# Performance work log

Measured on AMD Instinct MI355X. Metric: run time of the kernel, lower is better.

Reference implementation:

```python
import jax, jax.numpy as jnp
import numpy as np

IH, IW = 32, 32
HEADS, DIM_HEAD = 8, 32
EPS = 1e-6


def conv3x3(x, w):
    # x: [B,C,H,W], w: [O,I,3,3], stride 1, pad 1, no bias
    return jax.lax.conv_general_dilated(x, w, (1, 1), ((1, 1), (1, 1)),
                                        dimension_numbers=('NCHW', 'OIHW', 'NCHW'))


def groupnorm1(x, g, b):
    # GroupNorm(1, C): normalize over (C,H,W) per sample
    mu = jnp.mean(x, axis=(1, 2, 3), keepdims=True)
    var = jnp.var(x, axis=(1, 2, 3), keepdims=True)
    xn = (x - mu) * jax.lax.rsqrt(var + EPS)
    return xn * g[None, :, None, None] + b[None, :, None, None]


def proj(x, w, g, b):
    return jax.nn.gelu(groupnorm1(conv3x3(x, w), g, b), approximate=False)


def relative_index(ih, iw):
    coords = np.stack(np.meshgrid(np.arange(ih), np.arange(iw), indexing='ij')).reshape(2, -1)
    rel = coords[:, :, None] - coords[:, None, :]  # [2, n, n]
    rel[0] += ih - 1
    rel[1] += iw - 1
    rel[0] *= 2 * iw - 1
    return jnp.asarray(rel.sum(0).reshape(-1))  # [n*n]


def setup_inputs() -> dict:
    key = jax.random.key(0)
    ks = jax.random.split(key, 9)
    C = HEADS * DIM_HEAD  # 256
    B = 8
    s = 0.02
    inp = {
        'x': jax.random.normal(ks[0], (B, C, IH, IW), jnp.float32),
        'wq': jax.random.normal(ks[1], (C, C, 3, 3), jnp.float32) * s,
        'wk': jax.random.normal(ks[2], (C, C, 3, 3), jnp.float32) * s,
        'wv': jax.random.normal(ks[3], (C, C, 3, 3), jnp.float32) * s,
        'gq': jnp.ones((C,), jnp.float32), 'bq': jnp.zeros((C,), jnp.float32),
        'gk': jnp.ones((C,), jnp.float32), 'bk': jnp.zeros((C,), jnp.float32),
        'gv': jnp.ones((C,), jnp.float32), 'bv': jnp.zeros((C,), jnp.float32),
        'bias_table': jax.random.normal(ks[4], ((2 * IH - 1) * (2 * IW - 1), HEADS), jnp.float32) * s,
        'wo': jax.random.normal(ks[5], (C, C), jnp.float32) * s,
        'bo': jnp.zeros((C,), jnp.float32),
    }
    return inp


def reference(x, wq, wk, wv, gq, bq, gk, bk, gv, bv, bias_table, wo, bo):
    B, C, ih, iw = x.shape
    n = ih * iw
    h, d = HEADS, DIM_HEAD

    q = proj(x, wq, gq, bq)  # [B,C,H,W]
    k = proj(x, wk, gk, bk)
    v = proj(x, wv, gv, bv)

    # 'b c ih iw -> b (ih iw) c' then 'b n (h d) -> b h n d'  ==  [B,h,d,n] -> [B,h,n,d]
    def to_heads(t):
        return t.reshape(B, h, d, n).transpose(0, 1, 3, 2)

    q4, k4, v4 = to_heads(q), to_heads(k), to_heads(v)

    # NOTE: original code applies self.scale only when y is not None; y=None here -> no scale.
    dots = jnp.einsum('bhnd,bhmd->bhnm', q4, k4)  # [B,h,n,n]

    rel_idx = relative_index(ih, iw)  # [n*n]
    rel_bias = bias_table[rel_idx].reshape(n, n, h).transpose(2, 0, 1)[None]  # [1,h,n,n]

    attn = jax.nn.softmax(dots + rel_bias, axis=-1)
    out = jnp.einsum('bhnm,bhmd->bhnd', attn, v4)  # [B,h,n,d]

    # 'b h n d -> b n (h d)' then 'b (ih iw) c -> b c ih iw'
    out = out.transpose(0, 2, 1, 3).reshape(B, n, C).transpose(0, 2, 1).reshape(B, C, ih, iw)

    # to_out: 1x1 conv with bias (dropout=0 in eval)
    out = jnp.einsum('oc,bchw->bohw', wo, out) + bo[None, :, None, None]
    return out
```

## Files before the change

kernel.cpp:

```cpp
#include <hip/hip_runtime.h>
#include <cstdint>
#include <cstddef>

#define GEPS 1e-6f

using bf16x8 = __attribute__((ext_vector_type(8))) short;
using f32x4  = __attribute__((ext_vector_type(4))) float;

__device__ inline ushort f2bf(float x) {
    union { float f; uint32_t u; } v; v.f = x;
    uint32_t r = (v.u + 0x7fffu + ((v.u >> 16) & 1u)) >> 16;
    return (ushort)r;
}
__device__ inline float bf2f(ushort b) {
    union { float f; uint32_t u; } v; v.u = ((uint32_t)b) << 16;
    return v.f;
}

__device__ inline void gll16(const void* g, void* l) {
    __builtin_amdgcn_global_load_lds(
        (const __attribute__((address_space(1))) void*)g,
        (__attribute__((address_space(3))) void*)l, 16, 0, 0);
}

__global__ __launch_bounds__(256) void prep_k(
    const float* __restrict__ x,
    const float* __restrict__ wq, const float* __restrict__ wk,
    const float* __restrict__ wv, const float* __restrict__ wo,
    const float* __restrict__ btab,
    ushort* __restrict__ Ab, ushort* __restrict__ Wbuf,
    ushort* __restrict__ wo_bf, ushort* __restrict__ Bx)
{
    __shared__ __align__(16) ushort Xs[3 * 34 * 128];
    int tid = threadIdx.x;
    int blk = blockIdx.x;

    if (blk < 512) {
        int b = blk >> 6, py = (blk >> 1) & 31, half = blk & 1;
#pragma unroll
        for (int p = tid; p < 768; p += 256) {
            int yy = p >> 8;
            int q = p & 255;
            int col = (q >> 7) ? 33 : 0;
            int ci = q & 127;
            Xs[(yy * 34 + col) * 128 + ci] = 0;
        }
#pragma unroll
        for (int it = 0; it < 12; ++it) {
            int j = it * 256 + tid;
            int ci_l = j / 24;
            int o = (j - ci_l * 24) * 4;
            int yy = o >> 5, xx = o & 31;
            int row = py - 1 + yy;
            float4 v = make_float4(0.f, 0.f, 0.f, 0.f);
            if (row >= 0 && row < 32)
                v = *(const float4*)&x[((size_t)(b * 256 + half * 128 + ci_l)) * 1024 + row * 32 + xx];
            int base = (yy * 34 + xx + 1) * 128 + ci_l;
            Xs[base + 0 * 128] = f2bf(v.x);
            Xs[base + 1 * 128] = f2bf(v.y);
            Xs[base + 2 * 128] = f2bf(v.z);
            Xs[base + 3 * 128] = f2bf(v.w);
        }
        __syncthreads();
        ushort* dst = Ab + (size_t)(b * 1024 + py * 32) * 2304;
#pragma unroll
        for (int it = 0; it < 18; ++it) {
            int idx = it * 256 + tid;
            int ci8l = idx & 15;
            int tp = (idx >> 4) % 9;
            int px = idx / 144;
            int kh = tp / 3, kw = tp - kh * 3;
            uint4 p = *(const uint4*)&Xs[(kh * 34 + px + kw) * 128 + ci8l * 8];
            *(uint4*)&dst[(size_t)(px * 288 + tp * 32 + half * 16 + ci8l) * 8] = p;
        }
        return;
    }
    if (blk < 1280) {
        int wrow = blk - 512;
        int proj = wrow >> 8, co = wrow & 255;
        const float* src = ((proj == 0) ? wq : ((proj == 1) ? wk : wv)) + (size_t)co * 2304;
#pragma unroll
        for (int j = 0; j < 9; ++j) {
            int idx = j * 256 + tid;
            Xs[idx] = f2bf(src[idx]);
        }
        __syncthreads();
        ushort* dst = Wbuf + (size_t)wrow * 2304;
#pragma unroll
        for (int j = 0; j < 9; ++j)
            dst[j * 256 + tid] = Xs[tid * 9 + j];
        return;
    }
    if (blk < 1344) {
        int t = (blk - 1280) * 256 + tid;
        float4 v = *(const float4*)&wo[(size_t)t * 4];
        union { uint2 u; ushort s[4]; } o;
        o.s[0] = f2bf(v.x); o.s[1] = f2bf(v.y); o.s[2] = f2bf(v.z); o.s[3] = f2bf(v.w);
        *(uint2*)&wo_bf[(size_t)t * 4] = o.u;
        return;
    }
    int g = (blk - 1344) * 4 + (tid >> 6);
    int l = tid & 63;
    int h = g >> 10, qt = (g >> 4) & 63, kt = g & 15;
    int quad = l >> 4, c = l & 15;
    union { uint4 v[2]; ushort s[16]; } o;
#pragma unroll
    for (int f = 0; f < 4; ++f)
#pragma unroll
        for (int r = 0; r < 4; ++r) {
            int qrow = qt * 16 + quad * 4 + r;
            int key = kt * 64 + f * 16 + c;
            int dy = (qrow >> 5) - (key >> 5) + 31;
            int dx = (qrow & 31) - (key & 31) + 31;
            o.s[f * 4 + r] = f2bf(btab[(dy * 63 + dx) * 8 + h]);
        }
    uint4* dst = (uint4*)(Bx + ((size_t)g * 64 + l) * 16);
    dst[0] = o.v[0];
    dst[1] = o.v[1];
}

__global__ __launch_bounds__(256, 3) void gemm_bt(
    const ushort* __restrict__ A, const ushort* __restrict__ B,
    int M, int N, int K,
    ushort* __restrict__ Cpart,
    float* __restrict__ Cout, const float* __restrict__ bias, int mode)
{
    __shared__ __align__(16) ushort As[128 * 64];
    __shared__ __align__(16) ushort Bs[128 * 64];
    int tid = threadIdx.x;
    int mbase = blockIdx.x * 128, nbase = blockIdx.y * 128;
    int kspan = K / gridDim.z;
    int k0 = blockIdx.z * kspan;
    int wave = tid >> 6, lane = tid & 63;
    int wm = wave & 1, wn = wave >> 1;
    int quad = lane >> 4, c = lane & 15;

    int row_s = tid >> 3;
    int cc8 = (tid & 7) ^ (row_s & 7);
    ushort* ldsA = As + wave * 512;
    ushort* ldsB = Bs + wave * 512;

    f32x4 acc[4][4];
#pragma unroll
    for (int i = 0; i < 4; ++i)
#pragma unroll
        for (int j = 0; j < 4; ++j) acc[i][j] = (f32x4){0.f, 0.f, 0.f, 0.f};

    for (int kb = k0; kb < k0 + kspan; kb += 64) {
        __syncthreads();
#pragma unroll
        for (int R = 0; R < 4; ++R) {
            int row = R * 32 + row_s;
            gll16(A + (size_t)(mbase + row) * K + kb + cc8 * 8,
                  ldsA + R * 2048);
            gll16(B + (size_t)(nbase + row) * K + kb + cc8 * 8,
                  ldsB + R * 2048);
        }
        __syncthreads();
#pragma unroll
        for (int kq = 0; kq < 2; ++kq) {
            bf16x8 af[4], bfr[4];
            int sw = ((kq * 4 + quad) ^ (c & 7)) * 8;
#pragma unroll
            for (int i = 0; i < 4; ++i) {
                af[i]  = *(const bf16x8*)&As[(wm * 64 + i * 16 + c) * 64 + sw];
                bfr[i] = *(const bf16x8*)&Bs[(wn * 64 + i * 16 + c) * 64 + sw];
            }
#pragma unroll
            for (int i = 0; i < 4; ++i)
#pragma unroll
                for (int j = 0; j < 4; ++j)
                    acc[i][j] = __builtin_amdgcn_mfma_f32_16x16x32_bf16(
                        af[i], bfr[j], acc[i][j], 0, 0, 0);
        }
    }

    if (mode == 0) {
        ushort* Cp = Cpart + (size_t)blockIdx.z * M * N;
#pragma unroll
        for (int i = 0; i < 4; ++i) {
            int mrow = mbase + wm * 64 + i * 16 + quad * 4;
#pragma unroll
            for (int j = 0; j < 4; ++j) {
                int ncol = nbase + wn * 64 + j * 16 + c;
#pragma unroll
                for (int r = 0; r < 4; ++r)
                    Cp[(size_t)(mrow + r) * N + ncol] = f2bf(acc[i][j][r]);
            }
        }
    } else {
#pragma unroll
        for (int i = 0; i < 4; ++i) {
            int mrow0 = mbase + wm * 64 + i * 16 + quad * 4;
#pragma unroll
            for (int j = 0; j < 4; ++j) {
                int ncol = nbase + wn * 64 + j * 16 + c;
                int bb = ncol >> 10, px = ncol & 1023;
#pragma unroll
                for (int r = 0; r < 4; ++r) {
                    int o = mrow0 + r;
                    Cout[((size_t)bb * 256 + o) * 1024 + px] = acc[i][j][r] + bias[o];
                }
            }
        }
    }
}

__global__ __launch_bounds__(256) void stats1_k(const ushort* __restrict__ P0,
                                                const ushort* __restrict__ P1,
                                                float2* __restrict__ part)
{
    int t = blockIdx.x * 256 + threadIdx.x;
    size_t base = (size_t)t * 8;
    union { uint4 v; ushort s[8]; } a, b2;
    a.v  = *(const uint4*)&P0[base];
    b2.v = *(const uint4*)&P1[base];
    float s1 = 0.f, s2 = 0.f;
#pragma unroll
    for (int e = 0; e < 8; ++e) {
        float v = bf2f(a.s[e]) + bf2f(b2.s[e]);
        s1 += v; s2 += v * v;
    }
#pragma unroll
    for (int mk = 1; mk < 32; mk <<= 1) {
        s1 += __shfl_xor(s1, mk, 64);
        s2 += __shfl_xor(s2, mk, 64);
    }
    if ((threadIdx.x & 31) == 0) {
        int gg = t >> 5;
        int m = gg / 3;
        int proj = gg - m * 3;
        int b = m >> 10, slot = m & 1023;
        part[(proj * 8 + b) * 1024 + slot] = make_float2(s1, s2);
    }
}

__global__ __launch_bounds__(256) void stats2_k(const float2* __restrict__ part,
                                                float* __restrict__ stats)
{
    __shared__ float w1[4], w2[4];
    int s = blockIdx.x, tid = threadIdx.x;
    float s1 = 0.f, s2 = 0.f;
#pragma unroll
    for (int i = 0; i < 4; ++i) {
        float2 v = part[(size_t)s * 1024 + tid * 4 + i];
        s1 += v.x; s2 += v.y;
    }
#pragma unroll
    for (int mk = 1; mk < 64; mk <<= 1) {
        s1 += __shfl_xor(s1, mk, 64);
        s2 += __shfl_xor(s2, mk, 64);
    }
    if ((tid & 63) == 0) { w1[tid >> 6] = s1; w2[tid >> 6] = s2; }
    __syncthreads();
    if (tid == 0) {
        stats[s * 2 + 0] = w1[0] + w1[1] + w1[2] + w1[3];
        stats[s * 2 + 1] = w2[0] + w2[1] + w2[2] + w2[3];
    }
}

__global__ void gn_k(const ushort* __restrict__ P0, const ushort* __restrict__ P1,
                     const float* __restrict__ stats,
                     const float* __restrict__ gq, const float* __restrict__ bq,
                     const float* __restrict__ gk, const float* __restrict__ bk,
                     const float* __restrict__ gv, const float* __restrict__ bv,
                     ushort* __restrict__ qb, ushort* __restrict__ kb2,
                     ushort* __restrict__ vx)
{
    int t = blockIdx.x * 256 + threadIdx.x;
    int m = t / 96;
    int nn = (t - m * 96) * 8;
    int proj = nn >> 8, co = nn & 255;
    int b = m >> 10, px = m & 1023;
    float s1 = stats[(proj * 8 + b) * 2 + 0];
    float s2 = stats[(proj * 8 + b) * 2 + 1];
    const float Ninv = 1.f / 262144.f;
    float mu = s1 * Ninv;
    float var = fmaxf(s2 * Ninv - mu * mu, 0.f);
    float rsig = rsqrtf(var + GEPS);
    const float* gam = (proj == 0) ? gq : ((proj == 1) ? gk : gv);
    const float* bet = (proj == 0) ? bq : ((proj == 1) ? bk : bv);

    size_t base = (size_t)m * 768 + nn;
    union { uint4 v; ushort s[8]; } a, c2;
    a.v  = *(const uint4*)&P0[base];
    c2.v = *(const uint4*)&P1[base];
    union { uint4 v; ushort s[8]; } outp;
#pragma unroll
    for (int e = 0; e < 8; ++e) {
        int cc = co + e;
        float xv = bf2f(a.s[e]) + bf2f(c2.s[e]);
        float xn = (xv - mu) * rsig * gam[cc] + bet[cc];
        float ge = 0.5f * xn * (1.f + erff(xn * 0.70710678118654752f));
        outp.s[e] = f2bf(ge);
    }
    int h = co >> 5, d = co & 31;
    if (proj == 0) {
        *(uint4*)(qb + ((((size_t)b * 8 + h) * 1024 + px) * 32 + d)) = outp.v;
    } else if (proj == 1) {
        *(uint4*)(kb2 + ((((size_t)b * 8 + h) * 1024 + px) * 32 + d)) = outp.v;
    } else {
        ushort* vb = vx + ((size_t)b * 8 + h) * 32768;
        int kca = px >> 5, quad = (px >> 3) & 3, j = px & 7;
#pragma unroll
        for (int e = 0; e < 8; ++e) {
            int dd = d + e;
            vb[(((kca * 2 + (dd >> 4)) * 64) + quad * 16 + (dd & 15)) * 8 + j] = outp.s[e];
        }
    }
}

__global__ __launch_bounds__(256, 8) void attn_k(
    const ushort* __restrict__ qb, const ushort* __restrict__ kb,
    const ushort* __restrict__ vx, const ushort* __restrict__ Bx,
    ushort* __restrict__ Opart, float* __restrict__ lpart)
{
    __shared__ __align__(16) ushort Pl[4 * 16 * 72];
    int tid = threadIdx.x, wave = tid >> 6, lane = tid & 63;
    int quad = lane >> 4, c = lane & 15;
    int bh = blockIdx.y;
    int h = bh & 7;
    int z = blockIdx.z;
    int qbase = blockIdx.x * 64 + wave * 16;

    const ushort* Q  = qb + (size_t)bh * 1024 * 32;
    const ushort* Kp = kb + (size_t)bh * 1024 * 32;
    const ushort* Vb = vx + (size_t)bh * 32768;
    const ushort* bxp = Bx + (((size_t)(h * 64 + (qbase >> 4)) * 16) * 64 + lane) * 16;
    ushort* Pw = Pl + wave * 16 * 72;

    bf16x8 qf = *(const bf16x8*)&Q[(qbase + c) * 32 + quad * 8];

    float l_[4] = {0.f, 0.f, 0.f, 0.f};
    f32x4 Of0 = {0.f, 0.f, 0.f, 0.f}, Of1 = {0.f, 0.f, 0.f, 0.f};

    for (int kb64 = z * 512; kb64 < z * 512 + 512; kb64 += 64) {
        f32x4 S[4];
        f32x4 zf = {0.f, 0.f, 0.f, 0.f};
#pragma unroll
        for (int f = 0; f < 4; ++f) {
            bf16x8 kf = *(const bf16x8*)&Kp[(kb64 + f * 16 + c) * 32 + quad * 8];
            S[f] = __builtin_amdgcn_mfma_f32_16x16x32_bf16(qf, kf, zf, 0, 0, 0);
        }
        union { uint4 v[2]; ushort s[16]; } bu;
        const uint4* bsrc = (const uint4*)(bxp + (size_t)(kb64 >> 6) * 1024);
        bu.v[0] = bsrc[0];
        bu.v[1] = bsrc[1];
#pragma unroll
        for (int f = 0; f < 4; ++f)
#pragma unroll
            for (int r = 0; r < 4; ++r) {
                float p = __expf(S[f][r] + bf2f(bu.s[f * 4 + r]));
                S[f][r] = p;
                l_[r] += p;
            }
#pragma unroll
        for (int f = 0; f < 4; ++f)
#pragma unroll
            for (int r = 0; r < 4; ++r)
                Pw[(quad * 4 + r) * 72 + f * 16 + c] = f2bf(S[f][r]);
#pragma unroll
        for (int kc = 0; kc < 2; ++kc) {
            int kca = (kb64 >> 5) + kc;
            bf16x8 pf = *(const bf16x8*)&Pw[c * 72 + kc * 32 + quad * 8];
            bf16x8 vf0 = *(const bf16x8*)&Vb[((kca * 2 + 0) * 64 + lane) * 8];
            Of0 = __builtin_amdgcn_mfma_f32_16x16x32_bf16(pf, vf0, Of0, 0, 0, 0);
            bf16x8 vf1 = *(const bf16x8*)&Vb[((kca * 2 + 1) * 64 + lane) * 8];
            Of1 = __builtin_amdgcn_mfma_f32_16x16x32_bf16(pf, vf1, Of1, 0, 0, 0);
        }
    }
#pragma unroll
    for (int r = 0; r < 4; ++r) {
        float l = l_[r];
        l += __shfl_xor(l, 1, 64);
        l += __shfl_xor(l, 2, 64);
        l += __shfl_xor(l, 4, 64);
        l += __shfl_xor(l, 8, 64);
        int qr = qbase + quad * 4 + r;
        size_t ob = (((size_t)z * 64 + bh) * 1024 + qr) * 32;
        Opart[ob + c]      = f2bf(Of0[r]);
        Opart[ob + 16 + c] = f2bf(Of1[r]);
        if (c == 0) lpart[(size_t)z * 65536 + bh * 1024 + qr] = l;
    }
}

__global__ __launch_bounds__(256) void combine_k(const ushort* __restrict__ Opart,
                                                 const float* __restrict__ lpart,
                                                 ushort* __restrict__ attnout)
{
    int t = blockIdx.x * 256 + threadIdx.x;
    int g = t & 3;
    int qg = t >> 2;
    int bh = qg >> 10, qr = qg & 1023;
    int b = bh >> 3, h = bh & 7;
    size_t ob = ((size_t)qg) * 32 + g * 8;
    union { uint4 v; ushort s[8]; } o0, o1;
    o0.v = *(const uint4*)&Opart[ob];
    o1.v = *(const uint4*)&Opart[(size_t)64 * 1024 * 32 + ob];
    float inv = 1.f / (lpart[qg] + lpart[65536 + qg]);
    union { uint4 u; ushort s[8]; } o;
#pragma unroll
    for (int e = 0; e < 8; ++e)
        o.s[e] = f2bf((bf2f(o0.s[e]) + bf2f(o1.s[e])) * inv);
    *(uint4*)&attnout[(((size_t)b * 1024 + qr) * 256) + h * 32 + g * 8] = o.u;
}

extern "C" void kernel_launch(void* const* d_in, const int* in_sizes, int n_in,
                              void* d_out, int out_size, void* d_ws, size_t ws_size,
                              hipStream_t stream)
{
    const float* x    = (const float*)d_in[0];
    const float* wq   = (const float*)d_in[1];
    const float* wk   = (const float*)d_in[2];
    const float* wv   = (const float*)d_in[3];
    const float* gq   = (const float*)d_in[4];
    const float* bq   = (const float*)d_in[5];
    const float* gk   = (const float*)d_in[6];
    const float* bk   = (const float*)d_in[7];
    const float* gv   = (const float*)d_in[8];
    const float* bv   = (const float*)d_in[9];
    const float* btab = (const float*)d_in[10];
    const float* wo   = (const float*)d_in[11];
    const float* bo   = (const float*)d_in[12];
    float* out = (float*)d_out;

    char* w = (char*)d_ws;
    size_t off = 0;
    auto alloc = [&](size_t bytes) -> char* {
        char* p = w + off;
        off += (bytes + 255) & ~(size_t)255;
        return p;
    };
    ushort* Abuf    = (ushort*)alloc(8192ull * 2304 * 2);
    ushort* Wbuf    = (ushort*)alloc(768ull * 2304 * 2);
    ushort* wo_bf   = (ushort*)alloc(65536ull * 2);
    ushort* Bx      = (ushort*)alloc(8192ull * 64 * 16 * 2);
    ushort* P0      = (ushort*)alloc(8192ull * 768 * 2);
    ushort* P1      = (ushort*)alloc(8192ull * 768 * 2);
    float2* part    = (float2*)alloc(48ull * 1024 * 8);
    float*  stats   = (float*)alloc(384);
    ushort* Opart   = (ushort*)alloc(2ull * 64 * 1024 * 32 * 2);
    float*  lpart   = (float*)alloc(2ull * 64 * 1024 * 4);
    ushort* qb      = (ushort*)Abuf;
    ushort* kb2     = qb  + 8ull * 8 * 1024 * 32;
    ushort* vx      = kb2 + 8ull * 8 * 1024 * 32;
    ushort* attnout = vx  + 8ull * 8 * 32 * 1024;

    prep_k<<<3392, 256, 0, stream>>>(x, wq, wk, wv, wo, btab,
                                     Abuf, Wbuf, wo_bf, Bx);
    gemm_bt<<<dim3(64, 6, 2), 256, 0, stream>>>(Abuf, Wbuf, 8192, 768, 2304,
                                                P0, nullptr, nullptr, 0);
    stats1_k<<<3072, 256, 0, stream>>>(P0, P1, part);
    stats2_k<<<48, 256, 0, stream>>>(part, stats);
    gn_k<<<3072, 256, 0, stream>>>(P0, P1, stats, gq, bq, gk, bk, gv, bv,
                                   qb, kb2, vx);
    attn_k<<<dim3(16, 64, 2), 256, 0, stream>>>(qb, kb2, vx, Bx, Opart, lpart);
    combine_k<<<1024, 256, 0, stream>>>(Opart, lpart, attnout);
    gemm_bt<<<dim3(2, 64, 1), 256, 0, stream>>>(wo_bf, attnout, 256, 8192, 256,
                                                nullptr, out, bo, 1);
}
```

Before: 219.1 us.

## Fuse split-K attention combine into output projection GEMM and use exp2 softmax

Removes the separate combine kernel by having a dedicated output-projection GEMM load both attention partial outputs, normalize by the summed row sums, and write the bf16 tile straight into shared memory. This drops one launch and one round trip of the attention output through global memory. Separately, the relative bias is pre-scaled by log2(e) so the softmax uses a hardware exp2 with an FMA instead of __expf. The combine work now runs once per M-block, two times in total, and the B tile is loaded synchronously with no swizzle on the write side.

```diff
diff --git a/kernel.cpp b/kernel.cpp
--- a/kernel.cpp
+++ b/kernel.cpp
@@ -3,6 +3,7 @@
 #include <cstddef>
 
 #define GEPS 1e-6f
+#define LOG2E 1.44269504088896f
 
 using bf16x8 = __attribute__((ext_vector_type(8))) short;
 using f32x4  = __attribute__((ext_vector_type(4))) float;
@@ -112,7 +113,7 @@
             int key = kt * 64 + f * 16 + c;
             int dy = (qrow >> 5) - (key >> 5) + 31;
             int dx = (qrow & 31) - (key & 31) + 31;
-            o.s[f * 4 + r] = f2bf(btab[(dy * 63 + dx) * 8 + h]);
+            o.s[f * 4 + r] = f2bf(btab[(dy * 63 + dx) * 8 + h] * LOG2E);
         }
     uint4* dst = (uint4*)(Bx + ((size_t)g * 64 + l) * 16);
     dst[0] = o.v[0];
@@ -122,8 +123,7 @@
 __global__ __launch_bounds__(256, 3) void gemm_bt(
     const ushort* __restrict__ A, const ushort* __restrict__ B,
     int M, int N, int K,
-    ushort* __restrict__ Cpart,
-    float* __restrict__ Cout, const float* __restrict__ bias, int mode)
+    ushort* __restrict__ Cpart)
 {
     __shared__ __align__(16) ushort As[128 * 64];
     __shared__ __align__(16) ushort Bs[128 * 64];
@@ -175,33 +175,16 @@
         }
     }
 
-    if (mode == 0) {
-        ushort* Cp = Cpart + (size_t)blockIdx.z * M * N;
-#pragma unroll
-        for (int i = 0; i < 4; ++i) {
-            int mrow = mbase + wm * 64 + i * 16 + quad * 4;
-#pragma unroll
-            for (int j = 0; j < 4; ++j) {
-                int ncol = nbase + wn * 64 + j * 16 + c;
-#pragma unroll
-                for (int r = 0; r < 4; ++r)
-                    Cp[(size_t)(mrow + r) * N + ncol] = f2bf(acc[i][j][r]);
-            }
-        }
-    } else {
-#pragma unroll
-        for (int i = 0; i < 4; ++i) {
-            int mrow0 = mbase + wm * 64 + i * 16 + quad * 4;
-#pragma unroll
-            for (int j = 0; j < 4; ++j) {
-                int ncol = nbase + wn * 64 + j * 16 + c;
-                int bb = ncol >> 10, px = ncol & 1023;
-#pragma unroll
-                for (int r = 0; r < 4; ++r) {
-                    int o = mrow0 + r;
-                    Cout[((size_t)bb * 256 + o) * 1024 + px] = acc[i][j][r] + bias[o];
-                }
-            }
+    ushort* Cp = Cpart + (size_t)blockIdx.z * M * N;
+#pragma unroll
+    for (int i = 0; i < 4; ++i) {
+        int mrow = mbase + wm * 64 + i * 16 + quad * 4;
+#pragma unroll
+        for (int j = 0; j < 4; ++j) {
+            int ncol = nbase + wn * 64 + j * 16 + c;
+#pragma unroll
+            for (int r = 0; r < 4; ++r)
+                Cp[(size_t)(mrow + r) * N + ncol] = f2bf(acc[i][j][r]);
         }
     }
 }
@@ -350,7 +333,8 @@
         for (int f = 0; f < 4; ++f)
 #pragma unroll
             for (int r = 0; r < 4; ++r) {
-                float p = __expf(S[f][r] + bf2f(bu.s[f * 4 + r]));
+                float p = __builtin_amdgcn_exp2f(
+                    fmaf(S[f][r], LOG2E, bf2f(bu.s[f * 4 + r])));
                 S[f][r] = p;
                 l_[r] += p;
             }
@@ -384,25 +368,84 @@
     }
 }
 
-__global__ __launch_bounds__(256) void combine_k(const ushort* __restrict__ Opart,
-                                                 const float* __restrict__ lpart,
-                                                 ushort* __restrict__ attnout)
-{
-    int t = blockIdx.x * 256 + threadIdx.x;
-    int g = t & 3;
-    int qg = t >> 2;
-    int bh = qg >> 10, qr = qg & 1023;
-    int b = bh >> 3, h = bh & 7;
-    size_t ob = ((size_t)qg) * 32 + g * 8;
-    union { uint4 v; ushort s[8]; } o0, o1;
-    o0.v = *(const uint4*)&Opart[ob];
-    o1.v = *(const uint4*)&Opart[(size_t)64 * 1024 * 32 + ob];
-    float inv = 1.f / (lpart[qg] + lpart[65536 + qg]);
-    union { uint4 u; ushort s[8]; } o;
-#pragma unroll
-    for (int e = 0; e < 8; ++e)
-        o.s[e] = f2bf((bf2f(o0.s[e]) + bf2f(o1.s[e])) * inv);
-    *(uint4*)&attnout[(((size_t)b * 1024 + qr) * 256) + h * 32 + g * 8] = o.u;
+__global__ __launch_bounds__(256, 3) void oproj_k(
+    const ushort* __restrict__ Awo, const ushort* __restrict__ Opart,
+    const float* __restrict__ lpart,
+    float* __restrict__ Cout, const float* __restrict__ bias)
+{
+    __shared__ __align__(16) ushort As[128 * 64];
+    __shared__ __align__(16) ushort Bs[128 * 64];
+    int tid = threadIdx.x;
+    int mbase = blockIdx.x * 128, nbase = blockIdx.y * 128;
+    int wave = tid >> 6, lane = tid & 63;
+    int wm = wave & 1, wn = wave >> 1;
+    int quad = lane >> 4, c = lane & 15;
+
+    int row_s = tid >> 3;
+    int cc8 = (tid & 7) ^ (row_s & 7);
+    ushort* ldsA = As + wave * 512;
+
+    f32x4 acc[4][4];
+#pragma unroll
+    for (int i = 0; i < 4; ++i)
+#pragma unroll
+        for (int j = 0; j < 4; ++j) acc[i][j] = (f32x4){0.f, 0.f, 0.f, 0.f};
+
+    for (int kb = 0; kb < 256; kb += 64) {
+        __syncthreads();
+#pragma unroll
+        for (int R = 0; R < 4; ++R) {
+            int row = R * 32 + row_s;
+            gll16(Awo + (size_t)(mbase + row) * 256 + kb + cc8 * 8,
+                  ldsA + R * 2048);
+            int n = nbase + row;
+            int qr = n & 1023, bb = n >> 10;
+            int cb = (kb >> 3) + cc8;
+            int hh = cb >> 2, d0 = (cb & 3) * 8;
+            int qg = (bb * 8 + hh) * 1024 + qr;
+            union { uint4 v; ushort s[8]; } o0, o1;
+            o0.v = *(const uint4*)&Opart[(size_t)qg * 32 + d0];
+            o1.v = *(const uint4*)&Opart[2097152 + (size_t)qg * 32 + d0];
+            float inv = 1.f / (lpart[qg] + lpart[65536 + qg]);
+            union { uint4 v; ushort s[8]; } ob;
+#pragma unroll
+            for (int e = 0; e < 8; ++e)
+                ob.s[e] = f2bf((bf2f(o0.s[e]) + bf2f(o1.s[e])) * inv);
+            *(uint4*)&Bs[row * 64 + (tid & 7) * 8] = ob.v;
+        }
+        __syncthreads();
+#pragma unroll
+        for (int kq = 0; kq < 2; ++kq) {
+            bf16x8 af[4], bfr[4];
+            int sw = ((kq * 4 + quad) ^ (c & 7)) * 8;
+#pragma unroll
+            for (int i = 0; i < 4; ++i) {
+                af[i]  = *(const bf16x8*)&As[(wm * 64 + i * 16 + c) * 64 + sw];
+                bfr[i] = *(const bf16x8*)&Bs[(wn * 64 + i * 16 + c) * 64 + sw];
+            }
+#pragma unroll
+            for (int i = 0; i < 4; ++i)
+#pragma unroll
+                for (int j = 0; j < 4; ++j)
+                    acc[i][j] = __builtin_amdgcn_mfma_f32_16x16x32_bf16(
+                        af[i], bfr[j], acc[i][j], 0, 0, 0);
+        }
+    }
+
+#pragma unroll
+    for (int i = 0; i < 4; ++i) {
+        int mrow0 = mbase + wm * 64 + i * 16 + quad * 4;
+#pragma unroll
+        for (int j = 0; j < 4; ++j) {
+            int ncol = nbase + wn * 64 + j * 16 + c;
+            int bb = ncol >> 10, px = ncol & 1023;
+#pragma unroll
+            for (int r = 0; r < 4; ++r) {
+                int o = mrow0 + r;
+                Cout[((size_t)bb * 256 + o) * 1024 + px] = acc[i][j][r] + bias[o];
+            }
+        }
+    }
 }
 
 extern "C" void kernel_launch(void* const* d_in, const int* in_sizes, int n_in,
@@ -444,18 +487,14 @@
     ushort* qb      = (ushort*)Abuf;
     ushort* kb2     = qb  + 8ull * 8 * 1024 * 32;
     ushort* vx      = kb2 + 8ull * 8 * 1024 * 32;
-    ushort* attnout = vx  + 8ull * 8 * 32 * 1024;
 
     prep_k<<<3392, 256, 0, stream>>>(x, wq, wk, wv, wo, btab,
                                      Abuf, Wbuf, wo_bf, Bx);
-    gemm_bt<<<dim3(64, 6, 2), 256, 0, stream>>>(Abuf, Wbuf, 8192, 768, 2304,
-                                                P0, nullptr, nullptr, 0);
+    gemm_bt<<<dim3(64, 6, 2), 256, 0, stream>>>(Abuf, Wbuf, 8192, 768, 2304, P0);
     stats1_k<<<3072, 256, 0, stream>>>(P0, P1, part);
     stats2_k<<<48, 256, 0, stream>>>(part, stats);
     gn_k<<<3072, 256, 0, stream>>>(P0, P1, stats, gq, bq, gk, bk, gv, bv,
                                    qb, kb2, vx);
     attn_k<<<dim3(16, 64, 2), 256, 0, stream>>>(qb, kb2, vx, Bx, Opart, lpart);
-    combine_k<<<1024, 256, 0, stream>>>(Opart, lpart, attnout);
-    gemm_bt<<<dim3(2, 64, 1), 256, 0, stream>>>(wo_bf, attnout, 256, 8192, 256,
-                                                nullptr, out, bo, 1);
-}
+    oproj_k<<<dim3(2, 64), 256, 0, stream>>>(wo_bf, Opart, lpart, out, bo);
+}
```

After: 228.1 us. 4.1% more time.
